# Performance work log

Measured on AMD Instinct MI355X. Metric: run time of the kernel, lower is better.

Reference implementation:

```python
import jax, jax.numpy as jnp
import numpy as np

NUM_HEADS = 16

def rotate_half(x):
    h = x.shape[-1] // 2
    return jnp.concatenate([-x[..., h:], x[..., :h]], axis=-1)

def setup_inputs() -> dict:
    key = jax.random.key(0)
    ks = jax.random.split(key, 6)
    B, S, D, HD = 2, 2048, 2048, 128
    x = jax.random.normal(ks[0], (B, S, D), dtype=jnp.float32)
    # rotary tables for positions 0..S-1, per head_dim channel
    inv_freq = 1.0 / (10000.0 ** (jnp.arange(0, HD, 2, dtype=jnp.float32) / HD))
    t = jnp.arange(S, dtype=jnp.float32)
    freqs = jnp.outer(t, inv_freq)              # [S, HD/2]
    emb = jnp.concatenate([freqs, freqs], -1)   # [S, HD]
    cos = jnp.cos(emb)
    sin = jnp.sin(emb)
    scale = 0.02
    qkv_w = jax.random.normal(ks[1], (D, 3 * D), dtype=jnp.float32) * scale
    qkv_b = jnp.zeros((3 * D,), dtype=jnp.float32)
    out_w = jax.random.normal(ks[2], (D, D), dtype=jnp.float32) * scale
    out_b = jnp.zeros((D,), dtype=jnp.float32)
    return {"x": x, "cos": cos, "sin": sin, "qkv_w": qkv_w, "qkv_b": qkv_b,
            "out_w": out_w, "out_b": out_b}

def reference(x, cos, sin, qkv_w, qkv_b, out_w, out_b):
    B, S, D = x.shape
    H = NUM_HEADS
    HD = D // H
    qkv = x @ qkv_w + qkv_b                      # [B,S,3D]
    q, k, v = jnp.split(qkv, 3, axis=-1)
    def to_heads(t):
        return t.reshape(B, S, H, HD).transpose(0, 2, 1, 3)  # [B,H,S,HD]
    q, k, v = to_heads(q), to_heads(k), to_heads(v)
    # RoPE: cos/sin are [S,HD], broadcast over batch/head
    q = q * cos + rotate_half(q) * sin
    k = k * cos + rotate_half(k) * sin
    scores = jnp.einsum('bhqd,bhkd->bhqk', q, k) / jnp.sqrt(jnp.float32(HD))
    causal = jnp.tril(jnp.ones((S, S), dtype=bool))
    scores = jnp.where(causal, scores, jnp.finfo(scores.dtype).min)
    attn = jax.nn.softmax(scores, axis=-1)
    out = jnp.einsum('bhqk,bhkd->bhqd', attn, v)  # [B,H,S,HD]
    out = out.transpose(0, 2, 1, 3).reshape(B, S, D)
    return out @ out_w + out_b
```

## Files before the change

### kernel.cpp

```cpp
#include <hip/hip_runtime.h>
#include <cstddef>
#include <cstdint>

typedef __attribute__((ext_vector_type(8))) short bh8_t;
typedef __attribute__((ext_vector_type(4))) float f4_t;

__device__ __forceinline__ unsigned short f2bf(float x) {
    union { float f; unsigned u; } v; v.f = x;
    unsigned r = v.u + 0x7fffu + ((v.u >> 16) & 1u);
    return (unsigned short)(r >> 16);
}
__device__ __forceinline__ float bf2f(unsigned short u) {
    union { unsigned u; float f; } v; v.u = ((unsigned)u) << 16;
    return v.f;
}

__device__ __forceinline__ void gl_lds16(const void* g, void* l) {
    __builtin_amdgcn_global_load_lds(
        (const __attribute__((address_space(1))) unsigned int*)g,
        (__attribute__((address_space(3))) unsigned int*)l, 16, 0, 0);
}

#define B_    2
#define S_    2048
#define D_    2048
#define H_    16
#define HD_   128

__global__ __launch_bounds__(256) void cvt_f32_bf16(const float* __restrict__ in,
                                                    ushort* __restrict__ out) {
    size_t i = ((size_t)blockIdx.x * 256 + threadIdx.x) * 8;
    float4 a = *(const float4*)&in[i];
    float4 b = *(const float4*)&in[i + 4];
    ushort4 o0, o1;
    o0.x = f2bf(a.x); o0.y = f2bf(a.y); o0.z = f2bf(a.z); o0.w = f2bf(a.w);
    o1.x = f2bf(b.x); o1.y = f2bf(b.y); o1.z = f2bf(b.z); o1.w = f2bf(b.w);
    *(ushort4*)&out[i]     = o0;
    *(ushort4*)&out[i + 4] = o1;
}

__global__ __launch_bounds__(256) void transp_f32_bf16(const float* __restrict__ in,
                                                       ushort* __restrict__ out,
                                                       int R, int C) {
    __shared__ float T[64][68];
    const int t = threadIdx.x, rl = t >> 4, cl = t & 15;
    const int r0 = blockIdx.y * 64, c0 = blockIdx.x * 64;
    #pragma unroll
    for (int j = 0; j < 4; ++j) {
        int row = rl + 16 * j;
        float4 v = *(const float4*)&in[(size_t)(r0 + row) * C + c0 + cl * 4];
        *(float4*)&T[row][cl * 4] = v;
    }
    __syncthreads();
    #pragma unroll
    for (int j = 0; j < 4; ++j) {
        int row = rl + 16 * j;
        ushort4 o;
        o.x = f2bf(T[cl * 4 + 0][row]);
        o.y = f2bf(T[cl * 4 + 1][row]);
        o.z = f2bf(T[cl * 4 + 2][row]);
        o.w = f2bf(T[cl * 4 + 3][row]);
        *(ushort4*)&out[(size_t)(c0 + row) * R + r0 + cl * 4] = o;
    }
}

__global__ __launch_bounds__(256) void qkv_gemm(const ushort* __restrict__ A,
                                                const ushort* __restrict__ Bt,
                                                const float* __restrict__ bias,
                                                ushort* __restrict__ Qb,
                                                ushort* __restrict__ Kb,
                                                ushort* __restrict__ Vtg) {
    __shared__ ushort Al[128 * 32];
    __shared__ ushort Bl[128 * 32];
    const int tid = threadIdx.x;
    const int l = tid & 63, wv = tid >> 6;
    const int lr = l & 15, bk = l >> 4;
    const int wr = wv >> 1, wc = wv & 1;
    const int row0 = blockIdx.x * 128, col0 = blockIdx.y * 128;

    f4_t zero4 = {0.f, 0.f, 0.f, 0.f};
    f4_t acc[4][4];
    #pragma unroll
    for (int i = 0; i < 4; ++i)
        #pragma unroll
        for (int j = 0; j < 4; ++j) acc[i][j] = zero4;

    const int c0 = tid, c1 = tid + 256;
    const ushort* Ap0 = A  + (size_t)(row0 + (c0 >> 2)) * 2048 + (c0 & 3) * 8;
    const ushort* Ap1 = A  + (size_t)(row0 + (c1 >> 2)) * 2048 + (c1 & 3) * 8;
    const ushort* Bp0 = Bt + (size_t)(col0 + (c0 >> 2)) * 2048 + (c0 & 3) * 8;
    const ushort* Bp1 = Bt + (size_t)(col0 + (c1 >> 2)) * 2048 + (c1 & 3) * 8;
    ushort* Ad0 = Al + (size_t)(c0 - l) * 8;
    ushort* Ad1 = Al + (size_t)(c1 - l) * 8;
    ushort* Bd0 = Bl + (size_t)(c0 - l) * 8;
    ushort* Bd1 = Bl + (size_t)(c1 - l) * 8;

    for (int k0 = 0; k0 < 2048; k0 += 32) {
        gl_lds16(Ap0 + k0, Ad0);
        gl_lds16(Ap1 + k0, Ad1);
        gl_lds16(Bp0 + k0, Bd0);
        gl_lds16(Bp1 + k0, Bd1);
        __syncthreads();
        bh8_t af[4], bf[4];
        #pragma unroll
        for (int mf = 0; mf < 4; ++mf)
            af[mf] = *(const bh8_t*)&Al[(wr * 64 + mf * 16 + lr) * 32 + bk * 8];
        #pragma unroll
        for (int nf = 0; nf < 4; ++nf)
            bf[nf] = *(const bh8_t*)&Bl[(wc * 64 + nf * 16 + lr) * 32 + bk * 8];
        #pragma unroll
        for (int mf = 0; mf < 4; ++mf)
            #pragma unroll
            for (int nf = 0; nf < 4; ++nf)
                acc[mf][nf] = __builtin_amdgcn_mfma_f32_16x16x32_bf16(
                    af[mf], bf[nf], acc[mf][nf], 0, 0, 0);
        __syncthreads();
    }

    const int which = col0 >> 11;
    const int h = (col0 & 2047) >> 7;
    if (which < 2) {
        ushort* dst = which == 0 ? Qb : Kb;
        #pragma unroll
        for (int nf = 0; nf < 4; ++nf) {
            int n = col0 + wc * 64 + nf * 16 + lr;
            float bv = bias[n];
            int hd = (n & 2047) & 127;
            #pragma unroll
            for (int mf = 0; mf < 4; ++mf) {
                int mbase = row0 + wr * 64 + mf * 16 + bk * 4;
                #pragma unroll
                for (int r = 0; r < 4; ++r) {
                    int m = mbase + r;
                    int b = m >> 11, s = m & 2047;
                    dst[((size_t)(b * 16 + h) * 2048 + s) * 128 + hd] =
                        f2bf(acc[mf][nf][r] + bv);
                }
            }
        }
    } else {
        #pragma unroll
        for (int nf = 0; nf < 4; ++nf) {
            int n = col0 + wc * 64 + nf * 16 + lr;
            float bv = bias[n];
            int hd = n & 127;
            #pragma unroll
            for (int mf = 0; mf < 4; ++mf) {
                int mbase = row0 + wr * 64 + mf * 16 + bk * 4;
                int b = mbase >> 11, s4 = mbase & 2047;
                int spos = (s4 & ~31) | (((s4 >> 2) & 3) << 3) | (((s4 >> 4) & 1) << 2);
                ushort4 o;
                o.x = f2bf(acc[mf][nf][0] + bv);
                o.y = f2bf(acc[mf][nf][1] + bv);
                o.z = f2bf(acc[mf][nf][2] + bv);
                o.w = f2bf(acc[mf][nf][3] + bv);
                *(ushort4*)&Vtg[((size_t)((b * 16 + h) * 128 + hd)) * 2048 + spos] = o;
            }
        }
    }
}

__global__ __launch_bounds__(256) void rope_bf16(ushort* __restrict__ Qb,
                                                 ushort* __restrict__ Kb,
                                                 const float* __restrict__ cosn,
                                                 const float* __restrict__ sinn) {
    unsigned idx = blockIdx.x * 256 + threadIdx.x;
    int regn = idx >> 20;
    unsigned rest = idx & 1048575u;
    unsigned row = rest >> 4;
    int g = rest & 15;
    int s = row & 2047;
    ushort* base = (regn ? Kb : Qb) + (size_t)row * 128 + g * 4;
    uint2 lo = *(const uint2*)base;
    uint2 hi = *(const uint2*)(base + 64);
    float4 c4 = *(const float4*)&cosn[s * 128 + g * 4];
    float4 s4 = *(const float4*)&sinn[s * 128 + g * 4];
    const float sc = regn ? 1.0f : 0.08838834764831845f;
    const ushort* lp = (const ushort*)&lo;
    const ushort* hp = (const ushort*)&hi;
    float cf[4] = {c4.x, c4.y, c4.z, c4.w};
    float sf[4] = {s4.x, s4.y, s4.z, s4.w};
    ushort4 olo, ohi;
    ushort* olp = (ushort*)&olo;
    ushort* ohp = (ushort*)&ohi;
    #pragma unroll
    for (int e = 0; e < 4; ++e) {
        float lv = bf2f(lp[e]), hv = bf2f(hp[e]);
        olp[e] = f2bf((lv * cf[e] - hv * sf[e]) * sc);
        ohp[e] = f2bf((hv * cf[e] + lv * sf[e]) * sc);
    }
    *(ushort4*)base        = olo;
    *(ushort4*)(base + 64) = ohi;
}

__global__ __launch_bounds__(256) void attn2(const ushort* __restrict__ Qb,
                                             const ushort* __restrict__ Kb,
                                             const ushort* __restrict__ Vtg,
                                             ushort* __restrict__ AO) {
    __shared__ ushort lds[2][16384];
    const int tid = threadIdx.x;
    const int l = tid & 63, wq = tid >> 6;
    const int lr = l & 15, bk = l >> 4;
    const int id = blockIdx.x;
    const int bh = id & 31;
    const int qb = 31 - (id >> 5);
    const int q0 = qb * 64;
    const int qrow = q0 + wq * 16 + lr;
    const ushort* Qg = Qb + ((size_t)bh * 2048 + qrow) * 128;
    const ushort* KgB = Kb + (size_t)bh * 2048 * 128;
    const ushort* VgB = Vtg + (size_t)bh * 128 * 2048;

    bh8_t qf[4];
    #pragma unroll
    for (int ks = 0; ks < 4; ++ks)
        qf[ks] = *(const bh8_t*)(Qg + ks * 32 + bk * 8);

    float mrun = -1e30f, lrun = 0.f;
    f4_t zero4 = {0.f, 0.f, 0.f, 0.f};
    f4_t oacc[8];
    #pragma unroll
    for (int i = 0; i < 8; ++i) oacc[i] = zero4;

    auto issue = [&](int kt, int buf) {
        ushort* Kl = &lds[buf][0];
        ushort* Vl = &lds[buf][8192];
        const ushort* Kg = KgB + (size_t)kt * 64 * 128;
        #pragma unroll
        for (int i = 0; i < 4; ++i) {
            int c = tid + 256 * i;
            int key = c >> 4, d8 = (c & 15) ^ (key & 7);
            gl_lds16(Kg + key * 128 + d8 * 8, Kl + (size_t)(c - l) * 8);
        }
        #pragma unroll
        for (int i = 0; i < 4; ++i) {
            int c = tid + 256 * i;
            int d = c >> 3, p8 = (c & 7) ^ (d & 7);
            gl_lds16(VgB + (size_t)d * 2048 + kt * 64 + p8 * 8,
                     Vl + (size_t)(c - l) * 8);
        }
    };

    issue(0, 0);
    for (int kt = 0; kt <= qb; ++kt) {
        const int buf = kt & 1;
        if (kt < qb) {
            issue(kt + 1, buf ^ 1);
            asm volatile("s_waitcnt vmcnt(8)" ::: "memory");
        } else {
            asm volatile("s_waitcnt vmcnt(0)" ::: "memory");
        }
        __builtin_amdgcn_s_barrier();
        asm volatile("" ::: "memory");
        const char* Kl = (const char*)&lds[buf][0];
        const char* Vl = (const char*)&lds[buf][8192];

        f4_t sacc[4];
        #pragma unroll
        for (int kf = 0; kf < 4; ++kf) sacc[kf] = zero4;
        __builtin_amdgcn_s_setprio(1);
        #pragma unroll
        for (int ks = 0; ks < 4; ++ks)
            #pragma unroll
            for (int kf = 0; kf < 4; ++kf) {
                int key = kf * 16 + lr;
                int ab = (key * 256 + ks * 64 + bk * 16) ^ ((key & 7) << 4);
                bh8_t kv = *(const bh8_t*)(Kl + ab);
                sacc[kf] = __builtin_amdgcn_mfma_f32_16x16x32_bf16(
                    kv, qf[ks], sacc[kf], 0, 0, 0);
            }
        __builtin_amdgcn_s_setprio(0);

        if (kt == qb) {
            #pragma unroll
            for (int kf = 0; kf < 4; ++kf)
                #pragma unroll
                for (int r = 0; r < 4; ++r) {
                    int key = kt * 64 + kf * 16 + bk * 4 + r;
                    if (key > qrow) sacc[kf][r] = -1e30f;
                }
        }
        float mt = -1e30f;
        #pragma unroll
        for (int kf = 0; kf < 4; ++kf)
            #pragma unroll
            for (int r = 0; r < 4; ++r) mt = fmaxf(mt, sacc[kf][r]);
        mt = fmaxf(mt, __shfl_xor(mt, 16));
        mt = fmaxf(mt, __shfl_xor(mt, 32));
        float mnew = fmaxf(mrun, mt);
        float alpha = __expf(mrun - mnew);
        float rsum = 0.f;
        #pragma unroll
        for (int kf = 0; kf < 4; ++kf)
            #pragma unroll
            for (int r = 0; r < 4; ++r) {
                float p = __expf(sacc[kf][r] - mnew);
                sacc[kf][r] = p;
                rsum += p;
            }
        rsum += __shfl_xor(rsum, 16);
        rsum += __shfl_xor(rsum, 32);
        lrun = lrun * alpha + rsum;
        mrun = mnew;
        #pragma unroll
        for (int df = 0; df < 8; ++df) oacc[df] *= alpha;

        union { unsigned u[4]; bh8_t v; } bop[2];
        #pragma unroll
        for (int ks2 = 0; ks2 < 2; ++ks2)
            #pragma unroll
            for (int e = 0; e < 8; e += 2) {
                unsigned lo16 = f2bf(sacc[2 * ks2 + (e >> 2)][e & 3]);
                unsigned hi16 = f2bf(sacc[2 * ks2 + ((e + 1) >> 2)][(e + 1) & 3]);
                bop[ks2].u[e >> 1] = lo16 | (hi16 << 16);
            }
        __builtin_amdgcn_s_setprio(1);
        #pragma unroll
        for (int df = 0; df < 8; ++df) {
            int d = df * 16 + lr;
            #pragma unroll
            for (int ks2 = 0; ks2 < 2; ++ks2) {
                int ab = (d * 128 + ks2 * 64 + bk * 16) ^ ((d & 7) << 4);
                bh8_t av = *(const bh8_t*)(Vl + ab);
                oacc[df] = __builtin_amdgcn_mfma_f32_16x16x32_bf16(
                    av, bop[ks2].v, oacc[df], 0, 0, 0);
            }
        }
        __builtin_amdgcn_s_setprio(0);
        asm volatile("" ::: "memory");
        __builtin_amdgcn_s_barrier();
        asm volatile("" ::: "memory");
    }

    float inv = 1.0f / lrun;
    const int b = bh >> 4, h = bh & 15;
    #pragma unroll
    for (int df = 0; df < 8; ++df) {
        ushort4 o;
        o.x = f2bf(oacc[df][0] * inv);
        o.y = f2bf(oacc[df][1] * inv);
        o.z = f2bf(oacc[df][2] * inv);
        o.w = f2bf(oacc[df][3] * inv);
        size_t off = ((size_t)(b * 2048 + qrow)) * 2048 + h * 128 + df * 16 + bk * 4;
        *(ushort4*)&AO[off] = o;
    }
}

__global__ __launch_bounds__(256) void out_gemm(const ushort* __restrict__ A,
                                                const ushort* __restrict__ Bt,
                                                const float* __restrict__ bias,
                                                float* __restrict__ out) {
    __shared__ ushort Al[128 * 32];
    __shared__ ushort Bl[128 * 32];
    const int tid = threadIdx.x;
    const int l = tid & 63, wv = tid >> 6;
    const int lr = l & 15, bk = l >> 4;
    const int wr = wv >> 1, wc = wv & 1;
    const int row0 = blockIdx.x * 128, col0 = blockIdx.y * 128;

    f4_t zero4 = {0.f, 0.f, 0.f, 0.f};
    f4_t acc[4][4];
    #pragma unroll
    for (int i = 0; i < 4; ++i)
        #pragma unroll
        for (int j = 0; j < 4; ++j) acc[i][j] = zero4;

    const int c0 = tid, c1 = tid + 256;
    const ushort* Ap0 = A  + (size_t)(row0 + (c0 >> 2)) * 2048 + (c0 & 3) * 8;
    const ushort* Ap1 = A  + (size_t)(row0 + (c1 >> 2)) * 2048 + (c1 & 3) * 8;
    const ushort* Bp0 = Bt + (size_t)(col0 + (c0 >> 2)) * 2048 + (c0 & 3) * 8;
    const ushort* Bp1 = Bt + (size_t)(col0 + (c1 >> 2)) * 2048 + (c1 & 3) * 8;
    ushort* Ad0 = Al + (size_t)(c0 - l) * 8;
    ushort* Ad1 = Al + (size_t)(c1 - l) * 8;
    ushort* Bd0 = Bl + (size_t)(c0 - l) * 8;
    ushort* Bd1 = Bl + (size_t)(c1 - l) * 8;

    for (int k0 = 0; k0 < 2048; k0 += 32) {
        gl_lds16(Ap0 + k0, Ad0);
        gl_lds16(Ap1 + k0, Ad1);
        gl_lds16(Bp0 + k0, Bd0);
        gl_lds16(Bp1 + k0, Bd1);
        __syncthreads();
        bh8_t af[4], bf[4];
        #pragma unroll
        for (int mf = 0; mf < 4; ++mf)
            af[mf] = *(const bh8_t*)&Al[(wr * 64 + mf * 16 + lr) * 32 + bk * 8];
        #pragma unroll
        for (int nf = 0; nf < 4; ++nf)
            bf[nf] = *(const bh8_t*)&Bl[(wc * 64 + nf * 16 + lr) * 32 + bk * 8];
        #pragma unroll
        for (int mf = 0; mf < 4; ++mf)
            #pragma unroll
            for (int nf = 0; nf < 4; ++nf)
                acc[mf][nf] = __builtin_amdgcn_mfma_f32_16x16x32_bf16(
                    af[mf], bf[nf], acc[mf][nf], 0, 0, 0);
        __syncthreads();
    }

    #pragma unroll
    for (int nf = 0; nf < 4; ++nf) {
        int n = col0 + wc * 64 + nf * 16 + lr;
        float bv = bias[n];
        #pragma unroll
        for (int mf = 0; mf < 4; ++mf) {
            int mbase = row0 + wr * 64 + mf * 16 + bk * 4;
            #pragma unroll
            for (int r = 0; r < 4; ++r)
                out[(size_t)(mbase + r) * 2048 + n] = acc[mf][nf][r] + bv;
        }
    }
}

extern "C" void kernel_launch(void* const* d_in, const int* in_sizes, int n_in,
                              void* d_out, int out_size, void* d_ws, size_t ws_size,
                              hipStream_t stream)
{
    (void)in_sizes; (void)n_in; (void)out_size; (void)ws_size;
    const float* x     = (const float*)d_in[0];
    const float* cosn  = (const float*)d_in[1];
    const float* sinn  = (const float*)d_in[2];
    const float* qkv_w = (const float*)d_in[3];
    const float* qkv_b = (const float*)d_in[4];
    const float* out_w = (const float*)d_in[5];
    const float* out_b = (const float*)d_in[6];

    char* ws = (char*)d_ws;
    ushort* xb   = (ushort*)(ws);
    ushort* wtb  = (ushort*)(ws + ((size_t)16 << 20));
    ushort* owtb = (ushort*)(ws + ((size_t)40 << 20));
    ushort* Qb   = (ushort*)(ws + ((size_t)48 << 20));
    ushort* Kb   = (ushort*)(ws + ((size_t)64 << 20));
    ushort* Vtg  = (ushort*)(ws + ((size_t)80 << 20));
    ushort* AO   = (ushort*)(ws + ((size_t)96 << 20));

    hipLaunchKernelGGL(cvt_f32_bf16, dim3(4096), dim3(256), 0, stream, x, xb);
    hipLaunchKernelGGL(transp_f32_bf16, dim3(96, 32), dim3(256), 0, stream,
                       qkv_w, wtb, 2048, 6144);
    hipLaunchKernelGGL(transp_f32_bf16, dim3(32, 32), dim3(256), 0, stream,
                       out_w, owtb, 2048, 2048);
    hipLaunchKernelGGL(qkv_gemm, dim3(32, 48), dim3(256), 0, stream,
                       xb, wtb, qkv_b, Qb, Kb, Vtg);
    hipLaunchKernelGGL(rope_bf16, dim3(8192), dim3(256), 0, stream,
                       Qb, Kb, cosn, sinn);
    hipLaunchKernelGGL(attn2, dim3(1024), dim3(256), 0, stream,
                       Qb, Kb, Vtg, AO);
    hipLaunchKernelGGL(out_gemm, dim3(32, 16), dim3(256), 0, stream,
                       AO, owtb, out_b, (float*)d_out);
}
```

Baseline: 408.5 us.

## Double-buffer GEMM LDS loads and widen attention blocks to 128 queries

Both GEMMs now double-buffer their LDS tiles, prefetching the next K-slice with global_load_lds while MFMAs run on the current one. Explicit vmcnt waits and s_setprio replace the two __syncthreads per iteration. The attention kernel becomes 512-thread blocks covering 128 query rows, so each K/V tile loaded into LDS is shared by 8 waves instead of 4. Waves whose rows lie wholly above a key tile skip its compute under causal masking. The cost is doubled LDS use per GEMM block, a larger attention block that may lower occupancy, and uneven work across waves in the causal tail.

```diff
diff --git a/kernel.cpp b/kernel.cpp
--- a/kernel.cpp
+++ b/kernel.cpp
@@ -70,8 +70,8 @@
                                                 ushort* __restrict__ Qb,
                                                 ushort* __restrict__ Kb,
                                                 ushort* __restrict__ Vtg) {
-    __shared__ ushort Al[128 * 32];
-    __shared__ ushort Bl[128 * 32];
+    __shared__ ushort Al[2][128 * 32];
+    __shared__ ushort Bl[2][128 * 32];
     const int tid = threadIdx.x;
     const int l = tid & 63, wv = tid >> 6;
     const int lr = l & 15, bk = l >> 4;
@@ -90,31 +90,44 @@
     const ushort* Ap1 = A  + (size_t)(row0 + (c1 >> 2)) * 2048 + (c1 & 3) * 8;
     const ushort* Bp0 = Bt + (size_t)(col0 + (c0 >> 2)) * 2048 + (c0 & 3) * 8;
     const ushort* Bp1 = Bt + (size_t)(col0 + (c1 >> 2)) * 2048 + (c1 & 3) * 8;
-    ushort* Ad0 = Al + (size_t)(c0 - l) * 8;
-    ushort* Ad1 = Al + (size_t)(c1 - l) * 8;
-    ushort* Bd0 = Bl + (size_t)(c0 - l) * 8;
-    ushort* Bd1 = Bl + (size_t)(c1 - l) * 8;
-
+    const int d0 = (c0 - l) * 8, d1 = (c1 - l) * 8;
+
+    auto issue = [&](int k0, int buf) {
+        gl_lds16(Ap0 + k0, &Al[buf][d0]);
+        gl_lds16(Ap1 + k0, &Al[buf][d1]);
+        gl_lds16(Bp0 + k0, &Bl[buf][d0]);
+        gl_lds16(Bp1 + k0, &Bl[buf][d1]);
+    };
+
+    issue(0, 0);
     for (int k0 = 0; k0 < 2048; k0 += 32) {
-        gl_lds16(Ap0 + k0, Ad0);
-        gl_lds16(Ap1 + k0, Ad1);
-        gl_lds16(Bp0 + k0, Bd0);
-        gl_lds16(Bp1 + k0, Bd1);
-        __syncthreads();
+        const int buf = (k0 >> 5) & 1;
+        if (k0 + 32 < 2048) {
+            issue(k0 + 32, buf ^ 1);
+            asm volatile("s_waitcnt vmcnt(4)" ::: "memory");
+        } else {
+            asm volatile("s_waitcnt vmcnt(0)" ::: "memory");
+        }
+        __builtin_amdgcn_s_barrier();
+        asm volatile("" ::: "memory");
         bh8_t af[4], bf[4];
         #pragma unroll
         for (int mf = 0; mf < 4; ++mf)
-            af[mf] = *(const bh8_t*)&Al[(wr * 64 + mf * 16 + lr) * 32 + bk * 8];
+            af[mf] = *(const bh8_t*)&Al[buf][(wr * 64 + mf * 16 + lr) * 32 + bk * 8];
         #pragma unroll
         for (int nf = 0; nf < 4; ++nf)
-            bf[nf] = *(const bh8_t*)&Bl[(wc * 64 + nf * 16 + lr) * 32 + bk * 8];
+            bf[nf] = *(const bh8_t*)&Bl[buf][(wc * 64 + nf * 16 + lr) * 32 + bk * 8];
+        __builtin_amdgcn_s_setprio(1);
         #pragma unroll
         for (int mf = 0; mf < 4; ++mf)
             #pragma unroll
             for (int nf = 0; nf < 4; ++nf)
                 acc[mf][nf] = __builtin_amdgcn_mfma_f32_16x16x32_bf16(
                     af[mf], bf[nf], acc[mf][nf], 0, 0, 0);
-        __syncthreads();
+        __builtin_amdgcn_s_setprio(0);
+        asm volatile("" ::: "memory");
+        __builtin_amdgcn_s_barrier();
+        asm volatile("" ::: "memory");
     }
 
     const int which = col0 >> 11;
@@ -193,7 +206,7 @@
     *(ushort4*)(base + 64) = ohi;
 }
 
-__global__ __launch_bounds__(256) void attn2(const ushort* __restrict__ Qb,
+__global__ __launch_bounds__(512) void attn3(const ushort* __restrict__ Qb,
                                              const ushort* __restrict__ Kb,
                                              const ushort* __restrict__ Vtg,
                                              ushort* __restrict__ AO) {
@@ -203,8 +216,8 @@
     const int lr = l & 15, bk = l >> 4;
     const int id = blockIdx.x;
     const int bh = id & 31;
-    const int qb = 31 - (id >> 5);
-    const int q0 = qb * 64;
+    const int qb2 = 15 - (id >> 5);
+    const int q0 = qb2 * 128;
     const int qrow = q0 + wq * 16 + lr;
     const ushort* Qg = Qb + ((size_t)bh * 2048 + qrow) * 128;
     const ushort* KgB = Kb + (size_t)bh * 2048 * 128;
@@ -226,106 +239,110 @@
         ushort* Vl = &lds[buf][8192];
         const ushort* Kg = KgB + (size_t)kt * 64 * 128;
         #pragma unroll
-        for (int i = 0; i < 4; ++i) {
-            int c = tid + 256 * i;
+        for (int i = 0; i < 2; ++i) {
+            int c = tid + 512 * i;
             int key = c >> 4, d8 = (c & 15) ^ (key & 7);
             gl_lds16(Kg + key * 128 + d8 * 8, Kl + (size_t)(c - l) * 8);
         }
         #pragma unroll
-        for (int i = 0; i < 4; ++i) {
-            int c = tid + 256 * i;
+        for (int i = 0; i < 2; ++i) {
+            int c = tid + 512 * i;
             int d = c >> 3, p8 = (c & 7) ^ (d & 7);
             gl_lds16(VgB + (size_t)d * 2048 + kt * 64 + p8 * 8,
                      Vl + (size_t)(c - l) * 8);
         }
     };
 
+    const int nkt = 2 * qb2 + 2;
     issue(0, 0);
-    for (int kt = 0; kt <= qb; ++kt) {
+    for (int kt = 0; kt < nkt; ++kt) {
         const int buf = kt & 1;
-        if (kt < qb) {
+        if (kt + 1 < nkt) {
             issue(kt + 1, buf ^ 1);
-            asm volatile("s_waitcnt vmcnt(8)" ::: "memory");
+            asm volatile("s_waitcnt vmcnt(4)" ::: "memory");
         } else {
             asm volatile("s_waitcnt vmcnt(0)" ::: "memory");
         }
         __builtin_amdgcn_s_barrier();
         asm volatile("" ::: "memory");
-        const char* Kl = (const char*)&lds[buf][0];
-        const char* Vl = (const char*)&lds[buf][8192];
-
-        f4_t sacc[4];
-        #pragma unroll
-        for (int kf = 0; kf < 4; ++kf) sacc[kf] = zero4;
-        __builtin_amdgcn_s_setprio(1);
-        #pragma unroll
-        for (int ks = 0; ks < 4; ++ks)
-            #pragma unroll
-            for (int kf = 0; kf < 4; ++kf) {
-                int key = kf * 16 + lr;
-                int ab = (key * 256 + ks * 64 + bk * 16) ^ ((key & 7) << 4);
-                bh8_t kv = *(const bh8_t*)(Kl + ab);
-                sacc[kf] = __builtin_amdgcn_mfma_f32_16x16x32_bf16(
-                    kv, qf[ks], sacc[kf], 0, 0, 0);
+
+        if (kt * 64 <= q0 + wq * 16 + 15) {
+            const char* Kl = (const char*)&lds[buf][0];
+            const char* Vl = (const char*)&lds[buf][8192];
+
+            f4_t sacc[4];
+            #pragma unroll
+            for (int kf = 0; kf < 4; ++kf) sacc[kf] = zero4;
+            __builtin_amdgcn_s_setprio(1);
+            #pragma unroll
+            for (int ks = 0; ks < 4; ++ks)
+                #pragma unroll
+                for (int kf = 0; kf < 4; ++kf) {
+                    int key = kf * 16 + lr;
+                    int ab = (key * 256 + ks * 64 + bk * 16) ^ ((key & 7) << 4);
+                    bh8_t kv = *(const bh8_t*)(Kl + ab);
+                    sacc[kf] = __builtin_amdgcn_mfma_f32_16x16x32_bf16(
+                        kv, qf[ks], sacc[kf], 0, 0, 0);
+                }
+            __builtin_amdgcn_s_setprio(0);
+
+            if (kt * 64 + 63 > q0 + wq * 16) {
+                #pragma unroll
+                for (int kf = 0; kf < 4; ++kf)
+                    #pragma unroll
+                    for (int r = 0; r < 4; ++r) {
+                        int key = kt * 64 + kf * 16 + bk * 4 + r;
+                        if (key > qrow) sacc[kf][r] = -1e30f;
+                    }
             }
-        __builtin_amdgcn_s_setprio(0);
-
-        if (kt == qb) {
+            float mt = -1e30f;
             #pragma unroll
             for (int kf = 0; kf < 4; ++kf)
                 #pragma unroll
+                for (int r = 0; r < 4; ++r) mt = fmaxf(mt, sacc[kf][r]);
+            mt = fmaxf(mt, __shfl_xor(mt, 16));
+            mt = fmaxf(mt, __shfl_xor(mt, 32));
+            float mnew = fmaxf(mrun, mt);
+            float alpha = __expf(mrun - mnew);
+            float rsum = 0.f;
+            #pragma unroll
+            for (int kf = 0; kf < 4; ++kf)
+                #pragma unroll
                 for (int r = 0; r < 4; ++r) {
-                    int key = kt * 64 + kf * 16 + bk * 4 + r;
-                    if (key > qrow) sacc[kf][r] = -1e30f;
+                    float p = __expf(sacc[kf][r] - mnew);
+                    sacc[kf][r] = p;
+                    rsum += p;
                 }
-        }
-        float mt = -1e30f;
-        #pragma unroll
-        for (int kf = 0; kf < 4; ++kf)
-            #pragma unroll
-            for (int r = 0; r < 4; ++r) mt = fmaxf(mt, sacc[kf][r]);
-        mt = fmaxf(mt, __shfl_xor(mt, 16));
-        mt = fmaxf(mt, __shfl_xor(mt, 32));
-        float mnew = fmaxf(mrun, mt);
-        float alpha = __expf(mrun - mnew);
-        float rsum = 0.f;
-        #pragma unroll
-        for (int kf = 0; kf < 4; ++kf)
-            #pragma unroll
-            for (int r = 0; r < 4; ++r) {
-                float p = __expf(sacc[kf][r] - mnew);
-                sacc[kf][r] = p;
-                rsum += p;
+            rsum += __shfl_xor(rsum, 16);
+            rsum += __shfl_xor(rsum, 32);
+            lrun = lrun * alpha + rsum;
+            mrun = mnew;
+            #pragma unroll
+            for (int df = 0; df < 8; ++df) oacc[df] *= alpha;
+
+            union { unsigned u[4]; bh8_t v; } bop[2];
+            #pragma unroll
+            for (int ks2 = 0; ks2 < 2; ++ks2)
+                #pragma unroll
+                for (int e = 0; e < 8; e += 2) {
+                    unsigned lo16 = f2bf(sacc[2 * ks2 + (e >> 2)][e & 3]);
+                    unsigned hi16 = f2bf(sacc[2 * ks2 + ((e + 1) >> 2)][(e + 1) & 3]);
+                    bop[ks2].u[e >> 1] = lo16 | (hi16 << 16);
+                }
+            __builtin_amdgcn_s_setprio(1);
+            #pragma unroll
+            for (int df = 0; df < 8; ++df) {
+                int d = df * 16 + lr;
+                #pragma unroll
+                for (int ks2 = 0; ks2 < 2; ++ks2) {
+                    int ab = (d * 128 + ks2 * 64 + bk * 16) ^ ((d & 7) << 4);
+                    bh8_t av = *(const bh8_t*)(Vl + ab);
+                    oacc[df] = __builtin_amdgcn_mfma_f32_16x16x32_bf16(
+                        av, bop[ks2].v, oacc[df], 0, 0, 0);
+                }
             }
-        rsum += __shfl_xor(rsum, 16);
-        rsum += __shfl_xor(rsum, 32);
-        lrun = lrun * alpha + rsum;
-        mrun = mnew;
-        #pragma unroll
-        for (int df = 0; df < 8; ++df) oacc[df] *= alpha;
-
-        union { unsigned u[4]; bh8_t v; } bop[2];
-        #pragma unroll
-        for (int ks2 = 0; ks2 < 2; ++ks2)
-            #pragma unroll
-            for (int e = 0; e < 8; e += 2) {
-                unsigned lo16 = f2bf(sacc[2 * ks2 + (e >> 2)][e & 3]);
-                unsigned hi16 = f2bf(sacc[2 * ks2 + ((e + 1) >> 2)][(e + 1) & 3]);
-                bop[ks2].u[e >> 1] = lo16 | (hi16 << 16);
-            }
-        __builtin_amdgcn_s_setprio(1);
-        #pragma unroll
-        for (int df = 0; df < 8; ++df) {
-            int d = df * 16 + lr;
-            #pragma unroll
-            for (int ks2 = 0; ks2 < 2; ++ks2) {
-                int ab = (d * 128 + ks2 * 64 + bk * 16) ^ ((d & 7) << 4);
-                bh8_t av = *(const bh8_t*)(Vl + ab);
-                oacc[df] = __builtin_amdgcn_mfma_f32_16x16x32_bf16(
-                    av, bop[ks2].v, oacc[df], 0, 0, 0);
-            }
-        }
-        __builtin_amdgcn_s_setprio(0);
+            __builtin_amdgcn_s_setprio(0);
+        }
         asm volatile("" ::: "memory");
         __builtin_amdgcn_s_barrier();
         asm volatile("" ::: "memory");
@@ -349,8 +366,8 @@
                                                 const ushort* __restrict__ Bt,
                                                 const float* __restrict__ bias,
                                                 float* __restrict__ out) {
-    __shared__ ushort Al[128 * 32];
-    __shared__ ushort Bl[128 * 32];
+    __shared__ ushort Al[2][128 * 32];
+    __shared__ ushort Bl[2][128 * 32];
     const int tid = threadIdx.x;
     const int l = tid & 63, wv = tid >> 6;
     const int lr = l & 15, bk = l >> 4;
@@ -369,31 +386,44 @@
     const ushort* Ap1 = A  + (size_t)(row0 + (c1 >> 2)) * 2048 + (c1 & 3) * 8;
     const ushort* Bp0 = Bt + (size_t)(col0 + (c0 >> 2)) * 2048 + (c0 & 3) * 8;
     const ushort* Bp1 = Bt + (size_t)(col0 + (c1 >> 2)) * 2048 + (c1 & 3) * 8;
-    ushort* Ad0 = Al + (size_t)(c0 - l) * 8;
-    ushort* Ad1 = Al + (size_t)(c1 - l) * 8;
-    ushort* Bd0 = Bl + (size_t)(c0 - l) * 8;
-    ushort* Bd1 = Bl + (size_t)(c1 - l) * 8;
-
+    const int d0 = (c0 - l) * 8, d1 = (c1 - l) * 8;
+
+    auto issue = [&](int k0, int buf) {
+        gl_lds16(Ap0 + k0, &Al[buf][d0]);
+        gl_lds16(Ap1 + k0, &Al[buf][d1]);
+        gl_lds16(Bp0 + k0, &Bl[buf][d0]);
+        gl_lds16(Bp1 + k0, &Bl[buf][d1]);
+    };
+
+    issue(0, 0);
     for (int k0 = 0; k0 < 2048; k0 += 32) {
-        gl_lds16(Ap0 + k0, Ad0);
-        gl_lds16(Ap1 + k0, Ad1);
-        gl_lds16(Bp0 + k0, Bd0);
-        gl_lds16(Bp1 + k0, Bd1);
-        __syncthreads();
+        const int buf = (k0 >> 5) & 1;
+        if (k0 + 32 < 2048) {
+            issue(k0 + 32, buf ^ 1);
+            asm volatile("s_waitcnt vmcnt(4)" ::: "memory");
+        } else {
+            asm volatile("s_waitcnt vmcnt(0)" ::: "memory");
+        }
+        __builtin_amdgcn_s_barrier();
+        asm volatile("" ::: "memory");
         bh8_t af[4], bf[4];
         #pragma unroll
         for (int mf = 0; mf < 4; ++mf)
-            af[mf] = *(const bh8_t*)&Al[(wr * 64 + mf * 16 + lr) * 32 + bk * 8];
+            af[mf] = *(const bh8_t*)&Al[buf][(wr * 64 + mf * 16 + lr) * 32 + bk * 8];
         #pragma unroll
         for (int nf = 0; nf < 4; ++nf)
-            bf[nf] = *(const bh8_t*)&Bl[(wc * 64 + nf * 16 + lr) * 32 + bk * 8];
+            bf[nf] = *(const bh8_t*)&Bl[buf][(wc * 64 + nf * 16 + lr) * 32 + bk * 8];
+        __builtin_amdgcn_s_setprio(1);
         #pragma unroll
         for (int mf = 0; mf < 4; ++mf)
             #pragma unroll
             for (int nf = 0; nf < 4; ++nf)
                 acc[mf][nf] = __builtin_amdgcn_mfma_f32_16x16x32_bf16(
                     af[mf], bf[nf], acc[mf][nf], 0, 0, 0);
-        __syncthreads();
+        __builtin_amdgcn_s_setprio(0);
+        asm volatile("" ::: "memory");
+        __builtin_amdgcn_s_barrier();
+        asm volatile("" ::: "memory");
     }
 
     #pragma unroll
@@ -441,7 +471,7 @@
                        xb, wtb, qkv_b, Qb, Kb, Vtg);
     hipLaunchKernelGGL(rope_bf16, dim3(8192), dim3(256), 0, stream,
                        Qb, Kb, cosn, sinn);
-    hipLaunchKernelGGL(attn2, dim3(1024), dim3(256), 0, stream,
+    hipLaunchKernelGGL(attn3, dim3(512), dim3(512), 0, stream,
                        Qb, Kb, Vtg, AO);
     hipLaunchKernelGGL(out_gemm, dim3(32, 16), dim3(256), 0, stream,
                        AO, owtb, out_b, (float*)d_out);
```

Result: slower. 419.5 us (+2.7%).
